# Optimization experiments

Hardware: AMD Instinct MI355X
Metric: run time of the kernel (lower is better)

Reference implementation:

```python
import jax, jax.numpy as jnp
import numpy as np

T, HID = 2048, 1536
H, DK, DV = 12, 128, 128
KEY_DIM, VAL_DIM = H * DK, H * DV
CONV_K, GEN_RED = 4, 8
EPS = 1e-5


def setup_inputs() -> dict:
    key = jax.random.key(0)
    ks = jax.random.split(key, 12)
    def rn(k, sh, scale):
        return jax.random.normal(k, sh, dtype=jnp.float32) * scale
    inv = HID ** -0.5
    return {
        "hidden_states": rn(ks[0], (T, HID), 1.0),
        "Wq": rn(ks[1], (HID, KEY_DIM), inv),
        "Wk": rn(ks[2], (HID, KEY_DIM), inv),
        "Wv": rn(ks[3], (HID, VAL_DIM), inv),
        "Wb": rn(ks[4], (HID, H), inv),
        "Wa": rn(ks[5], (HID, H), inv),
        "A_log": jnp.log(jax.random.uniform(ks[6], (H,), minval=1e-3, maxval=16.0)),
        "dt_bias": jnp.ones((H,), jnp.float32),
        "Wg1": rn(ks[7], (HID, HID // GEN_RED), inv),
        "Wg2": rn(ks[8], (HID // GEN_RED, VAL_DIM * CONV_K), (HID // GEN_RED) ** -0.5),
        "Wgate": rn(ks[9], (HID, VAL_DIM), inv),
        "norm_weight": jnp.ones((DV,), jnp.float32),
        "Wo": rn(ks[10], (VAL_DIM, HID), VAL_DIM ** -0.5),
    }


def _dynamic_conv(v, hs, Wg1, Wg2):
    # per-token per-channel causal depthwise conv; kernels generated from hidden_states
    w = jax.nn.silu(hs @ Wg1) @ Wg2                    # (T, VAL_DIM*K)
    w = w.reshape(T, VAL_DIM, CONV_K)                  # (T, D, K)
    vpad = jnp.pad(v, ((CONV_K - 1, 0), (0, 0)))       # causal left pad
    windows = jnp.stack([vpad[i:i + T] for i in range(CONV_K)], axis=1)  # (T, K, D)
    return jax.nn.silu(jnp.einsum('tkd,tdk->td', windows, w))


def _gated_delta_rule(q, k, v, g, beta):
    # q,k: (T,H,DK); v: (T,H,DV); g,beta: (T,H)
    scale = DK ** -0.5
    def step(S, inp):
        q_t, k_t, v_t, g_t, b_t = inp
        S = S * jnp.exp(g_t)[:, None, None]            # decay state
        kv = jnp.einsum('hk,hkv->hv', k_t, S)          # k^T S
        S = S + jnp.einsum('hk,hv->hkv', k_t, (v_t - kv) * b_t[:, None])
        o_t = jnp.einsum('hk,hkv->hv', q_t, S) * scale
        return S, o_t
    S0 = jnp.zeros((H, DK, DV), jnp.float32)
    _, o = jax.lax.scan(step, S0, (q, k, v, g, beta))
    return o                                           # (T, H, DV)


def reference(hidden_states, Wq, Wk, Wv, Wb, Wa, A_log, dt_bias,
              Wg1, Wg2, Wgate, norm_weight, Wo):
    hs = hidden_states
    q = jax.nn.silu(hs @ Wq).reshape(T, H, DK)
    k = jax.nn.silu(hs @ Wk).reshape(T, H, DK)
    v = _dynamic_conv(hs @ Wv, hs, Wg1, Wg2).reshape(T, H, DV)
    beta = jax.nn.sigmoid(hs @ Wb)                           # (T, H)
    g = -jnp.exp(A_log) * jax.nn.softplus(hs @ Wa + dt_bias)  # (T, H) log-decay
    o = _gated_delta_rule(q, k, v, g, beta)                  # (T, H, DV)
    # gated RMSNorm over head_v_dim
    gate = (hs @ Wgate).reshape(T, H, DV)
    o = o * jax.lax.rsqrt(jnp.mean(o * o, axis=-1, keepdims=True) + EPS)
    o = o * norm_weight * (gate * jax.nn.sigmoid(gate))
    return o.reshape(T, VAL_DIM) @ Wo
```

## Files before the change

kernel.cpp:

```cpp
#include <hip/hip_runtime.h>
#include <hip/hip_bf16.h>
#include <math.h>

#define T     2048
#define HID   1536
#define NH    12
#define DK    128
#define DV    128
#define CONVK 4
#define CH    64
#define NC    32

typedef __attribute__((ext_vector_type(8))) short bf16x8;
typedef __attribute__((ext_vector_type(8))) _Float16 fp16x8;
typedef __attribute__((ext_vector_type(4))) float floatx4;

__device__ __forceinline__ float siluf(float x) {
    return x / (1.0f + __expf(-x));
}
__device__ __forceinline__ unsigned short f2bf(float f) {
    union { __hip_bfloat16 b; unsigned short u; } cv;
    cv.b = __float2bfloat16(f);
    return cv.u;
}
__device__ __forceinline__ float bf2f(unsigned short u) {
    union { unsigned int u; float f; } cv;
    cv.u = ((unsigned int)u) << 16;
    return cv.f;
}
__device__ __forceinline__ unsigned short f2h(float f) {
    union { _Float16 h; unsigned short u; } cv;
    cv.h = (_Float16)f;
    return cv.u;
}
__device__ __forceinline__ void gl_lds16(const void* g, void* l) {
    __builtin_amdgcn_global_load_lds(
        (const __attribute__((address_space(1))) void*)g,
        (__attribute__((address_space(3))) void*)l, 16, 0, 0);
}
__device__ __forceinline__ void split8_store(const float* xv,
                                             unsigned short* dh, unsigned short* dl) {
    ushort4 h0, h1, l0, l1;
    h0.x = f2bf(xv[0]); l0.x = f2bf(xv[0] - bf2f(h0.x));
    h0.y = f2bf(xv[1]); l0.y = f2bf(xv[1] - bf2f(h0.y));
    h0.z = f2bf(xv[2]); l0.z = f2bf(xv[2] - bf2f(h0.z));
    h0.w = f2bf(xv[3]); l0.w = f2bf(xv[3] - bf2f(h0.w));
    h1.x = f2bf(xv[4]); l1.x = f2bf(xv[4] - bf2f(h1.x));
    h1.y = f2bf(xv[5]); l1.y = f2bf(xv[5] - bf2f(h1.y));
    h1.z = f2bf(xv[6]); l1.z = f2bf(xv[6] - bf2f(h1.z));
    h1.w = f2bf(xv[7]); l1.w = f2bf(xv[7] - bf2f(h1.w));
    *(ushort4*)dh = h0; *(ushort4*)(dh + 4) = h1;
    *(ushort4*)dl = l0; *(ushort4*)(dl + 4) = l1;
}

__global__ __launch_bounds__(256) void splitcast3_kernel(const float* __restrict__ s,
                                                         unsigned short* __restrict__ hi,
                                                         unsigned short* __restrict__ lo,
                                                         unsigned short* __restrict__ h16,
                                                         int n4) {
    int i = blockIdx.x * 256 + threadIdx.x;
    if (i >= n4) return;
    float4 x = ((const float4*)s)[i];
    ushort4 h, l, f;
    h.x = f2bf(x.x); l.x = f2bf(x.x - bf2f(h.x)); f.x = f2h(x.x);
    h.y = f2bf(x.y); l.y = f2bf(x.y - bf2f(h.y)); f.y = f2h(x.y);
    h.z = f2bf(x.z); l.z = f2bf(x.z - bf2f(h.z)); f.z = f2h(x.z);
    h.w = f2bf(x.w); l.w = f2bf(x.w - bf2f(h.w)); f.w = f2h(x.w);
    ((ushort4*)hi)[i] = h;
    ((ushort4*)lo)[i] = l;
    ((ushort4*)h16)[i] = f;
}

__global__ __launch_bounds__(256) void transsplit_kernel(const float* __restrict__ src,
                                                         unsigned short* __restrict__ hi,
                                                         unsigned short* __restrict__ lo,
                                                         int K, int N) {
    __shared__ float tile[32][33];
    const int k0 = blockIdx.y * 32, n0 = blockIdx.x * 32;
    const int tx = threadIdx.x, ty = threadIdx.y;
#pragma unroll
    for (int r = 0; r < 4; ++r) {
        int kk = k0 + ty + 8 * r, nn = n0 + tx;
        tile[ty + 8 * r][tx] = (nn < N) ? src[(size_t)kk * N + nn] : 0.0f;
    }
    __syncthreads();
#pragma unroll
    for (int r = 0; r < 4; ++r) {
        int nn = n0 + ty + 8 * r, kk = k0 + tx;
        if (nn < N) {
            float x = tile[tx][ty + 8 * r];
            unsigned short h = f2bf(x);
            hi[(size_t)nn * K + kk] = h;
            lo[(size_t)nn * K + kk] = f2bf(x - bf2f(h));
        }
    }
}

__global__ __launch_bounds__(256) void transcasth_kernel(const float* __restrict__ src,
                                                         unsigned short* __restrict__ dst,
                                                         int K, int N) {
    __shared__ float tile[32][33];
    const int k0 = blockIdx.y * 32, n0 = blockIdx.x * 32;
    const int tx = threadIdx.x, ty = threadIdx.y;
#pragma unroll
    for (int r = 0; r < 4; ++r) {
        int kk = k0 + ty + 8 * r, nn = n0 + tx;
        tile[ty + 8 * r][tx] = (nn < N) ? src[(size_t)kk * N + nn] : 0.0f;
    }
    __syncthreads();
#pragma unroll
    for (int r = 0; r < 4; ++r) {
        int nn = n0 + ty + 8 * r, kk = k0 + tx;
        if (nn < N) dst[(size_t)nn * K + kk] = f2h(tile[tx][ty + 8 * r]);
    }
}

template<int EPI, int MODE>
__global__ __launch_bounds__(256)
void mgemm(const unsigned short* __restrict__ Ah, const unsigned short* __restrict__ Al,
           const unsigned short* __restrict__ Bh, const unsigned short* __restrict__ Bl,
           int K, int N, float* __restrict__ C, unsigned short* __restrict__ Cb,
           float* __restrict__ qf, float* __restrict__ vf, float* __restrict__ kf,
           unsigned short* __restrict__ gsilb, unsigned short* __restrict__ w1h16,
           float* __restrict__ bgraw)
{
    constexpr int BN   = MODE ? 64 : 128;
    constexpr int BCH  = BN / 16;
    constexpr int NFR  = MODE ? 2 : 4;
    __shared__ unsigned short AsH[2][4096];
    __shared__ unsigned short BsH[2][BCH * 512];
    __shared__ unsigned short AsL[MODE ? 2 : 1][MODE ? 4096 : 4];
    __shared__ unsigned short BsL[MODE ? 2 : 1][MODE ? BCH * 512 : 4];
    const int tid = threadIdx.x;
    const int wave = tid >> 6, lane = tid & 63;
    const int wr = wave >> 1, wc = wave & 1;
    const int lm = lane & 15, lq = lane >> 4;
    const int rowBase = blockIdx.y * 128, colBase = blockIdx.x * BN;

    floatx4 acc[4][NFR];
#pragma unroll
    for (int i = 0; i < 4; ++i)
#pragma unroll
        for (int j = 0; j < NFR; ++j) acc[i][j] = (floatx4){0.f, 0.f, 0.f, 0.f};

    const int mt0 = wave * 2, mt1 = wave * 2 + 1;
    const size_t aOff0 = (size_t)(rowBase + mt0 * 16 + lm) * K + lq * 8;
    const size_t aOff1 = (size_t)(rowBase + mt1 * 16 + lm) * K + lq * 8;
    const size_t bOff0 = (size_t)(colBase + mt0 * 16 + lm) * K + lq * 8;
    const size_t bOff1 = (size_t)(colBase + mt1 * 16 + lm) * K + lq * 8;
    const size_t bOffW = (size_t)(colBase + wave * 16 + lm) * K + lq * 8;

    auto STAGE = [&](int buf, int k0) {
        gl_lds16(Ah + aOff0 + k0, &AsH[buf][mt0 * 512]);
        gl_lds16(Ah + aOff1 + k0, &AsH[buf][mt1 * 512]);
        if (MODE) {
            gl_lds16(Al + aOff0 + k0, &AsL[buf][mt0 * 512]);
            gl_lds16(Al + aOff1 + k0, &AsL[buf][mt1 * 512]);
            gl_lds16(Bh + bOffW + k0, &BsH[buf][wave * 512]);
            gl_lds16(Bl + bOffW + k0, &BsL[buf][wave * 512]);
        } else {
            gl_lds16(Bh + bOff0 + k0, &BsH[buf][mt0 * 512]);
            gl_lds16(Bh + bOff1 + k0, &BsH[buf][mt1 * 512]);
        }
    };

    const int nIter = K >> 5;
    STAGE(0, 0);
    __syncthreads();
    int cur = 0;
    for (int it = 0; it < nIter; ++it) {
        if (it + 1 < nIter) STAGE(cur ^ 1, (it + 1) << 5);
        if (MODE == 0) {
            fp16x8 a[4], b[4];
#pragma unroll
            for (int i = 0; i < 4; ++i) {
                a[i] = *(const fp16x8*)&AsH[cur][(wr * 4 + i) * 512 + lane * 8];
                b[i] = *(const fp16x8*)&BsH[cur][(wc * 4 + i) * 512 + lane * 8];
            }
#pragma unroll
            for (int mi = 0; mi < 4; ++mi)
#pragma unroll
                for (int ni = 0; ni < 4; ++ni)
                    acc[mi][ni] = __builtin_amdgcn_mfma_f32_16x16x32_f16(
                        a[mi], b[ni], acc[mi][ni], 0, 0, 0);
        } else {
            bf16x8 ah[4], al[4], bh[2], bl[2];
#pragma unroll
            for (int i = 0; i < 4; ++i) {
                ah[i] = *(const bf16x8*)&AsH[cur][(wr * 4 + i) * 512 + lane * 8];
                al[i] = *(const bf16x8*)&AsL[cur][(wr * 4 + i) * 512 + lane * 8];
            }
#pragma unroll
            for (int j = 0; j < 2; ++j) {
                bh[j] = *(const bf16x8*)&BsH[cur][(wc * 2 + j) * 512 + lane * 8];
                bl[j] = *(const bf16x8*)&BsL[cur][(wc * 2 + j) * 512 + lane * 8];
            }
#pragma unroll
            for (int mi = 0; mi < 4; ++mi)
#pragma unroll
                for (int ni = 0; ni < 2; ++ni) {
                    acc[mi][ni] = __builtin_amdgcn_mfma_f32_16x16x32_bf16(
                        ah[mi], bh[ni], acc[mi][ni], 0, 0, 0);
                    acc[mi][ni] = __builtin_amdgcn_mfma_f32_16x16x32_bf16(
                        al[mi], bh[ni], acc[mi][ni], 0, 0, 0);
                    acc[mi][ni] = __builtin_amdgcn_mfma_f32_16x16x32_bf16(
                        ah[mi], bl[ni], acc[mi][ni], 0, 0, 0);
                }
        }
        __syncthreads();
        cur ^= 1;
    }

#pragma unroll
    for (int mi = 0; mi < 4; ++mi)
#pragma unroll
        for (int ni = 0; ni < NFR; ++ni) {
            const int col = colBase + wc * (NFR * 16) + ni * 16 + lm;
#pragma unroll
            for (int r = 0; r < 4; ++r) {
                const int row = rowBase + wr * 64 + mi * 16 + lq * 4 + r;
                const float x = acc[mi][ni][r];
                if (EPI == 0) {
                    C[(size_t)row * N + col] = x;
                } else if (EPI == 3) {
                    Cb[(size_t)row * N + col] = f2bf(x);
                } else if (EPI == 1) {
                    if (col < 1536)       qf[(size_t)row * 1536 + col] = siluf(x);
                    else if (col < 3072)  vf[(size_t)row * 1536 + col - 1536] = x;
                    else if (col < 4608)  gsilb[(size_t)row * 1536 + col - 3072] = f2bf(siluf(x));
                    else if (col < 4800)  w1h16[(size_t)row * 192 + col - 4608] = f2h(siluf(x));
                } else {
                    if (col < 1536)       kf[(size_t)row * 1536 + col] = siluf(x);
                    else if (col < 1560)  bgraw[(size_t)row * 24 + col - 1536] = x;
                }
            }
        }
}

__global__ __launch_bounds__(256) void bg2_kernel(const float* __restrict__ bgraw,
                                                  const float* __restrict__ A_log,
                                                  const float* __restrict__ dt_bias,
                                                  float* __restrict__ beta,
                                                  float* __restrict__ g) {
    int idx = blockIdx.x * 256 + threadIdx.x;
    if (idx >= T * 24) return;
    int t = idx / 24, c = idx % 24;
    float x = bgraw[idx];
    if (c < 12) {
        beta[t * NH + c] = 1.0f / (1.0f + __expf(-x));
    } else {
        int h = c - 12;
        float y = x + dt_bias[h];
        float sp = (y > 20.0f) ? y : log1pf(__expf(y));
        g[t * NH + h] = -__expf(A_log[h]) * sp;
    }
}

__global__ __launch_bounds__(256) void conv_kernel(const float* __restrict__ vpre,
                                                   const unsigned short* __restrict__ w,
                                                   float* __restrict__ v) {
    const int idx = blockIdx.x * 256 + threadIdx.x;
    if (idx >= T * HID) return;
    const int t = idx / HID, d = idx % HID;
    const ushort4 wv = *(const ushort4*)(w + (size_t)t * (HID * CONVK) + d * 4);
    const float w4[4] = { bf2f(wv.x), bf2f(wv.y), bf2f(wv.z), bf2f(wv.w) };
    float acc = 0.0f;
#pragma unroll
    for (int i = 0; i < CONVK; i++) {
        const int ts = t - (CONVK - 1) + i;
        if (ts >= 0) acc += vpre[(size_t)ts * HID + d] * w4[i];
    }
    v[idx] = siluf(acc);
}

__global__ __launch_bounds__(256) void prep_kernel(
    const float* __restrict__ q, const float* __restrict__ k,
    unsigned short* __restrict__ Qth, unsigned short* __restrict__ Qtl,
    unsigned short* __restrict__ Kth, unsigned short* __restrict__ Ktl)
{
    __shared__ float KT[128 * 68];
    const int c = blockIdx.x, h = blockIdx.y;
    const int tid = threadIdx.x;
    const size_t tb = (size_t)(h * NC + c) * 8192;

    {
        const int li = tid >> 2, lq4 = tid & 3;
        const float* src = k + (size_t)(c * CH + li) * HID + h * DK + lq4 * 32;
#pragma unroll
        for (int f = 0; f < 8; ++f) {
            float4 x = *(const float4*)(src + f * 4);
            int d0 = lq4 * 32 + f * 4;
            KT[(d0 + 0) * 68 + li] = x.x; KT[(d0 + 1) * 68 + li] = x.y;
            KT[(d0 + 2) * 68 + li] = x.z; KT[(d0 + 3) * 68 + li] = x.w;
        }
    }

#pragma unroll
    for (int e = 0; e < 4; ++e) {
        int u = e * 256 + tid;
        int ch = u >> 6, l = u & 63;
        int i = (ch >> 2) * 16 + (l & 15);
        int dbase = (ch & 3) * 32 + (l >> 4) * 8;
        const float* src = q + (size_t)(c * CH + i) * HID + h * DK + dbase;
        float4 a = *(const float4*)src, b = *(const float4*)(src + 4);
        float xv[8] = {a.x, a.y, a.z, a.w, b.x, b.y, b.z, b.w};
        split8_store(xv, &Qth[tb + ch * 512 + l * 8], &Qtl[tb + ch * 512 + l * 8]);
    }
    __syncthreads();

#pragma unroll
    for (int e = 0; e < 4; ++e) {
        int u = e * 256 + tid;
        int ch = u >> 6, l = u & 63;
        int dk = (ch >> 1) * 16 + (l & 15);
        int ibase = (ch & 1) * 32 + (l >> 4) * 8;
        float4 a = *(const float4*)&KT[dk * 68 + ibase];
        float4 b = *(const float4*)&KT[dk * 68 + ibase + 4];
        float xv[8] = {a.x, a.y, a.z, a.w, b.x, b.y, b.z, b.w};
        split8_store(xv, &Kth[tb + ch * 512 + l * 8], &Ktl[tb + ch * 512 + l * 8]);
    }
}

__global__ __launch_bounds__(256, 1) void chunkloc_kernel(
    const float* __restrict__ q, const float* __restrict__ k, const float* __restrict__ v,
    const float* __restrict__ g, const float* __restrict__ beta,
    float* __restrict__ X1g,
    unsigned short* __restrict__ X2th, unsigned short* __restrict__ X2tl,
    float* __restrict__ Mg, float* __restrict__ csg)
{
    __shared__ unsigned short KhS[64 * 136], KlS[64 * 136];
    __shared__ unsigned short QhS[64 * 136], QlS[64 * 136];
    __shared__ float KT[128 * 68];
    __shared__ float Vs[64 * 132];
    __shared__ float As[64 * 68];
    __shared__ float cs[64], sb[64], sbb[64];

    const int c = blockIdx.x, h = blockIdx.y;
    const int tid = threadIdx.x;
    const int wave = tid >> 6, lane = tid & 63;
    const int lm = lane & 15, lq = lane >> 4;
    const int li = tid >> 2, lq4 = tid & 3;
    const size_t rowbase = (size_t)(c * CH) * HID + h * DK;

    {
        const float* ksrc = k + rowbase + (size_t)li * HID + lq4 * 32;
        const float* qsrc = q + rowbase + (size_t)li * HID + lq4 * 32;
        const float* vsrc = v + (size_t)(c * CH + li) * HID + h * DV + lq4 * 32;
#pragma unroll
        for (int f = 0; f < 8; ++f) {
            float4 kx = *(const float4*)(ksrc + f * 4);
            float4 qx = *(const float4*)(qsrc + f * 4);
            float4 vx = *(const float4*)(vsrc + f * 4);
            const int d0 = lq4 * 32 + f * 4;
            {
                ushort4 hh, ll;
                hh.x = f2bf(kx.x); ll.x = f2bf(kx.x - bf2f(hh.x));
                hh.y = f2bf(kx.y); ll.y = f2bf(kx.y - bf2f(hh.y));
                hh.z = f2bf(kx.z); ll.z = f2bf(kx.z - bf2f(hh.z));
                hh.w = f2bf(kx.w); ll.w = f2bf(kx.w - bf2f(hh.w));
                *(ushort4*)&KhS[li * 136 + d0] = hh;
                *(ushort4*)&KlS[li * 136 + d0] = ll;
            }
            {
                ushort4 hh, ll;
                hh.x = f2bf(qx.x); ll.x = f2bf(qx.x - bf2f(hh.x));
                hh.y = f2bf(qx.y); ll.y = f2bf(qx.y - bf2f(hh.y));
                hh.z = f2bf(qx.z); ll.z = f2bf(qx.z - bf2f(hh.z));
                hh.w = f2bf(qx.w); ll.w = f2bf(qx.w - bf2f(hh.w));
                *(ushort4*)&QhS[li * 136 + d0] = hh;
                *(ushort4*)&QlS[li * 136 + d0] = ll;
            }
            KT[(d0 + 0) * 68 + li] = kx.x;
            KT[(d0 + 1) * 68 + li] = kx.y;
            KT[(d0 + 2) * 68 + li] = kx.z;
            KT[(d0 + 3) * 68 + li] = kx.w;
            *(float4*)&Vs[li * 132 + d0] = vx;
        }
    }
    if (tid < 64) {
        float gv = g[(c * CH + tid) * NH + h];
        float bv = beta[(c * CH + tid) * NH + h];
        float csv = gv;
#pragma unroll
        for (int off = 1; off < 64; off <<= 1) {
            float n = __shfl_up(csv, off);
            if (tid >= off) csv += n;
        }
        cs[tid] = csv; sb[tid] = bv; sbb[tid] = bv * __expf(csv);
    }
    __syncthreads();

    {
        const int ti = wave;
#pragma unroll
        for (int tj = 0; tj < 4; ++tj) {
            floatx4 acc = (floatx4){0.f, 0.f, 0.f, 0.f};
#pragma unroll
            for (int ks = 0; ks < 4; ++ks) {
                bf16x8 a_h = *(const bf16x8*)&KhS[(ti * 16 + lm) * 136 + ks * 32 + lq * 8];
                bf16x8 a_l = *(const bf16x8*)&KlS[(ti * 16 + lm) * 136 + ks * 32 + lq * 8];
                bf16x8 b_h = *(const bf16x8*)&KhS[(tj * 16 + lm) * 136 + ks * 32 + lq * 8];
                bf16x8 b_l = *(const bf16x8*)&KlS[(tj * 16 + lm) * 136 + ks * 32 + lq * 8];
                acc = __builtin_amdgcn_mfma_f32_16x16x32_bf16(a_h, b_h, acc, 0, 0, 0);
                acc = __builtin_amdgcn_mfma_f32_16x16x32_bf16(a_h, b_l, acc, 0, 0, 0);
                acc = __builtin_amdgcn_mfma_f32_16x16x32_bf16(a_l, b_h, acc, 0, 0, 0);
            }
#pragma unroll
            for (int r = 0; r < 4; ++r) {
                const int i = ti * 16 + lq * 4 + r, j = tj * 16 + lm;
                As[i * 68 + j] = (j < i) ? sb[i] * __expf(cs[i] - cs[j]) * acc[r] : 0.0f;
            }
        }
        const size_t mbase = (size_t)(h * NC + c) * CH * CH;
#pragma unroll
        for (int tj = 0; tj < 4; ++tj) {
            floatx4 acc = (floatx4){0.f, 0.f, 0.f, 0.f};
#pragma unroll
            for (int ks = 0; ks < 4; ++ks) {
                bf16x8 a_h = *(const bf16x8*)&QhS[(ti * 16 + lm) * 136 + ks * 32 + lq * 8];
                bf16x8 a_l = *(const bf16x8*)&QlS[(ti * 16 + lm) * 136 + ks * 32 + lq * 8];
                bf16x8 b_h = *(const bf16x8*)&KhS[(tj * 16 + lm) * 136 + ks * 32 + lq * 8];
                bf16x8 b_l = *(const bf16x8*)&KlS[(tj * 16 + lm) * 136 + ks * 32 + lq * 8];
                acc = __builtin_amdgcn_mfma_f32_16x16x32_bf16(a_h, b_h, acc, 0, 0, 0);
                acc = __builtin_amdgcn_mfma_f32_16x16x32_bf16(a_h, b_l, acc, 0, 0, 0);
                acc = __builtin_amdgcn_mfma_f32_16x16x32_bf16(a_l, b_h, acc, 0, 0, 0);
            }
#pragma unroll
            for (int r = 0; r < 4; ++r) {
                const int i = ti * 16 + lq * 4 + r, j = tj * 16 + lm;
                Mg[mbase + (size_t)i * 64 + j] =
                    (j <= i) ? __expf(cs[i] - cs[j]) * acc[r] : 0.0f;
            }
        }
    }

    float xc[64];
    const int col = tid;
    if (col < 128) {
#pragma unroll
        for (int i = 0; i < 64; ++i) xc[i] = sb[i] * Vs[i * 132 + col];
    } else {
        const int dcol = col - 128;
#pragma unroll
        for (int i4 = 0; i4 < 16; ++i4) {
            float4 kq = *(const float4*)&KT[dcol * 68 + i4 * 4];
            xc[i4 * 4 + 0] = sbb[i4 * 4 + 0] * kq.x;
            xc[i4 * 4 + 1] = sbb[i4 * 4 + 1] * kq.y;
            xc[i4 * 4 + 2] = sbb[i4 * 4 + 2] * kq.z;
            xc[i4 * 4 + 3] = sbb[i4 * 4 + 3] * kq.w;
        }
    }
    __syncthreads();

#pragma unroll
    for (int i = 1; i < 64; ++i) {
        float a = xc[i];
#pragma unroll
        for (int j4 = 0; j4 < (i + 3) / 4; ++j4) {
            float4 a4 = *(const float4*)&As[i * 68 + j4 * 4];
            a -= a4.x * xc[j4 * 4 + 0] + a4.y * xc[j4 * 4 + 1]
               + a4.z * xc[j4 * 4 + 2] + a4.w * xc[j4 * 4 + 3];
        }
        xc[i] = a;
    }

    {
        const size_t xbase = (size_t)(h * NC + c) * CH * 128;
        if (col < 128) {
            for (int i = 0; i < 64; ++i) X1g[xbase + (size_t)i * 128 + col] = xc[i];
        } else {
            for (int i = 0; i < 64; ++i) Vs[i * 132 + (col - 128)] = xc[i];
        }
    }
    if (tid < 64) csg[(size_t)(h * NC + c) * CH + tid] = cs[tid];
    __syncthreads();

    {
        const size_t tb = (size_t)(h * NC + c) * 8192;
#pragma unroll
        for (int e = 0; e < 4; ++e) {
            int u = e * 256 + tid;
            int ch = u >> 6, l = u & 63;
            int i = (ch >> 2) * 16 + (l & 15);
            int dbase = (ch & 3) * 32 + (l >> 4) * 8;
            float4 a = *(const float4*)&Vs[i * 132 + dbase];
            float4 b = *(const float4*)&Vs[i * 132 + dbase + 4];
            float xv[8] = {-a.x, -a.y, -a.z, -a.w, -b.x, -b.y, -b.z, -b.w};
            split8_store(xv, &X2th[tb + ch * 512 + l * 8], &X2tl[tb + ch * 512 + l * 8]);
        }
    }
}

struct StFrags {
    bf16x8 xh[4], xl[4], qh[4], ql[4], kh[4], kl[4];
    float x1r[4], csr[4], cs63;
};

__device__ __forceinline__ void st_load(
    StFrags& f,
    const unsigned short* __restrict__ Qth, const unsigned short* __restrict__ Qtl,
    const unsigned short* __restrict__ Kth, const unsigned short* __restrict__ Ktl,
    const unsigned short* __restrict__ X2th, const unsigned short* __restrict__ X2tl,
    const float* __restrict__ X1g, const float* __restrict__ csg,
    int h, int c, int db, int mw, int lane, int lq, int lm)
{
    const size_t hc = (size_t)(h * NC + c);
    const size_t xb = hc * CH * 128;
    const size_t tb = hc * 8192 + (size_t)lane * 8;
#pragma unroll
    for (int ks = 0; ks < 4; ++ks) {
        const size_t off = tb + (size_t)(mw * 4 + ks) * 512;
        f.xh[ks] = *(const bf16x8*)(X2th + off);
        f.xl[ks] = *(const bf16x8*)(X2tl + off);
        f.qh[ks] = *(const bf16x8*)(Qth + off);
        f.ql[ks] = *(const bf16x8*)(Qtl + off);
        f.kh[ks] = *(const bf16x8*)(Kth + off);
        f.kl[ks] = *(const bf16x8*)(Ktl + off);
    }
#pragma unroll
    for (int r = 0; r < 4; ++r) {
        const int row = mw * 16 + lq * 4 + r;
        f.x1r[r] = X1g[xb + (size_t)row * 128 + db * 16 + lm];
        f.csr[r] = csg[hc * CH + row];
    }
    f.cs63 = csg[hc * CH + 63];
}

__device__ __forceinline__ void st_compute(
    const StFrags& f, floatx4& st0, floatx4& st1,
    unsigned short* SBh, unsigned short* SBl,
    unsigned short* UBh, unsigned short* UBl,
    float* __restrict__ X1g, float* __restrict__ o,
    int h, int c, int db, int mw, int lane, int lq, int lm)
{
    const size_t hc = (size_t)(h * NC + c);
    const size_t xb = hc * CH * 128;

    {
        floatx4 aU0 = (floatx4){0.f, 0.f, 0.f, 0.f};
        floatx4 aU1 = (floatx4){0.f, 0.f, 0.f, 0.f};
        floatx4 aO0 = (floatx4){0.f, 0.f, 0.f, 0.f};
        floatx4 aO1 = (floatx4){0.f, 0.f, 0.f, 0.f};
#pragma unroll
        for (int ks = 0; ks < 4; ++ks) {
            bf16x8 sh = *(const bf16x8*)&SBh[lm * 136 + ks * 32 + lq * 8];
            bf16x8 sl = *(const bf16x8*)&SBl[lm * 136 + ks * 32 + lq * 8];
            if (ks & 1) {
                aU1 = __builtin_amdgcn_mfma_f32_16x16x32_bf16(f.xh[ks], sh, aU1, 0, 0, 0);
                aU1 = __builtin_amdgcn_mfma_f32_16x16x32_bf16(f.xh[ks], sl, aU1, 0, 0, 0);
                aU1 = __builtin_amdgcn_mfma_f32_16x16x32_bf16(f.xl[ks], sh, aU1, 0, 0, 0);
                aO1 = __builtin_amdgcn_mfma_f32_16x16x32_bf16(f.qh[ks], sh, aO1, 0, 0, 0);
                aO1 = __builtin_amdgcn_mfma_f32_16x16x32_bf16(f.qh[ks], sl, aO1, 0, 0, 0);
                aO1 = __builtin_amdgcn_mfma_f32_16x16x32_bf16(f.ql[ks], sh, aO1, 0, 0, 0);
            } else {
                aU0 = __builtin_amdgcn_mfma_f32_16x16x32_bf16(f.xh[ks], sh, aU0, 0, 0, 0);
                aU0 = __builtin_amdgcn_mfma_f32_16x16x32_bf16(f.xh[ks], sl, aU0, 0, 0, 0);
                aU0 = __builtin_amdgcn_mfma_f32_16x16x32_bf16(f.xl[ks], sh, aU0, 0, 0, 0);
                aO0 = __builtin_amdgcn_mfma_f32_16x16x32_bf16(f.qh[ks], sh, aO0, 0, 0, 0);
                aO0 = __builtin_amdgcn_mfma_f32_16x16x32_bf16(f.qh[ks], sl, aO0, 0, 0, 0);
                aO0 = __builtin_amdgcn_mfma_f32_16x16x32_bf16(f.ql[ks], sh, aO0, 0, 0, 0);
            }
        }
#pragma unroll
        for (int r = 0; r < 4; ++r) {
            const int row = mw * 16 + lq * 4 + r;
            const float u = aU0[r] + aU1[r] + f.x1r[r];
            X1g[xb + (size_t)row * 128 + db * 16 + lm] = u;
            const float up = u * __expf(f.cs63 - f.csr[r]);
            unsigned short uh = f2bf(up);
            UBh[lm * 72 + row] = uh;
            UBl[lm * 72 + row] = f2bf(up - bf2f(uh));
            o[(size_t)(c * CH + row) * HID + h * DV + db * 16 + lm] =
                __expf(f.csr[r]) * (aO0[r] + aO1[r]);
        }
    }
    __syncthreads();

    {
        const float bC = __expf(f.cs63);
#pragma unroll
        for (int mt2 = 0; mt2 < 2; ++mt2) {
            const int mt = mw * 2 + mt2;
            floatx4 acc;
            floatx4 stc = mt2 ? st1 : st0;
#pragma unroll
            for (int r = 0; r < 4; ++r) acc[r] = bC * stc[r];
#pragma unroll
            for (int ks = 0; ks < 2; ++ks) {
                bf16x8 ah = f.kh[mt2 * 2 + ks];
                bf16x8 al = f.kl[mt2 * 2 + ks];
                bf16x8 bh = *(const bf16x8*)&UBh[lm * 72 + ks * 32 + lq * 8];
                bf16x8 bl = *(const bf16x8*)&UBl[lm * 72 + ks * 32 + lq * 8];
                acc = __builtin_amdgcn_mfma_f32_16x16x32_bf16(ah, bh, acc, 0, 0, 0);
                acc = __builtin_amdgcn_mfma_f32_16x16x32_bf16(ah, bl, acc, 0, 0, 0);
                acc = __builtin_amdgcn_mfma_f32_16x16x32_bf16(al, bh, acc, 0, 0, 0);
            }
            if (mt2) st1 = acc; else st0 = acc;
            ushort4 shv, slv;
#pragma unroll
            for (int r = 0; r < 4; ++r) {
                const float sv = acc[r];
                unsigned short sh = f2bf(sv);
                ((unsigned short*)&shv)[r] = sh;
                ((unsigned short*)&slv)[r] = f2bf(sv - bf2f(sh));
            }
            const int dkb = mt * 16 + lq * 4;
            *(ushort4*)&SBh[lm * 136 + dkb] = shv;
            *(ushort4*)&SBl[lm * 136 + dkb] = slv;
        }
    }
    __syncthreads();
}

__global__ __launch_bounds__(256, 1) void state_kernel(
    const unsigned short* __restrict__ Qth, const unsigned short* __restrict__ Qtl,
    const unsigned short* __restrict__ Kth, const unsigned short* __restrict__ Ktl,
    const unsigned short* __restrict__ X2th, const unsigned short* __restrict__ X2tl,
    float* __restrict__ X1g ,
    const float* __restrict__ csg, float* __restrict__ o)
{
    __shared__ unsigned short SBh[16 * 136], SBl[16 * 136];
    __shared__ unsigned short UBh[16 * 72],  UBl[16 * 72];

    const int h = blockIdx.x, db = blockIdx.y;
    const int tid = threadIdx.x;
    const int mw = tid >> 6, lane = tid & 63;
    const int lm = lane & 15, lq = lane >> 4;

    for (int idx = tid; idx < 16 * 136; idx += 256) { SBh[idx] = 0; SBl[idx] = 0; }
    floatx4 st0 = (floatx4){0.f, 0.f, 0.f, 0.f};
    floatx4 st1 = (floatx4){0.f, 0.f, 0.f, 0.f};
    __syncthreads();

    StFrags fA, fB;
    st_load(fA, Qth, Qtl, Kth, Ktl, X2th, X2tl, X1g, csg, h, 0, db, mw, lane, lq, lm);
    for (int c = 0; c < NC; c += 2) {
        st_load(fB, Qth, Qtl, Kth, Ktl, X2th, X2tl, X1g, csg, h, c + 1, db, mw, lane, lq, lm);
        __builtin_amdgcn_sched_barrier(0);
        st_compute(fA, st0, st1, SBh, SBl, UBh, UBl, X1g, o, h, c, db, mw, lane, lq, lm);
        if (c + 2 < NC)
            st_load(fA, Qth, Qtl, Kth, Ktl, X2th, X2tl, X1g, csg, h, c + 2, db, mw, lane, lq, lm);
        __builtin_amdgcn_sched_barrier(0);
        st_compute(fB, st0, st1, SBh, SBl, UBh, UBl, X1g, o, h, c + 1, db, mw, lane, lq, lm);
    }
}

__global__ __launch_bounds__(256) void outk_kernel(
    const float* __restrict__ Ug, const float* __restrict__ Mg,
    float* __restrict__ o)
{
    __shared__ float Msh[64 * 68];
    __shared__ float Ush[64 * 68];

    const int c = blockIdx.x, h = blockIdx.y;
    const int dvb = blockIdx.z * 64;
    const int tid = threadIdx.x;
    const size_t hc = (size_t)(h * NC + c);

    for (int e = 0; e < 16; ++e) {
        int idx = e * 256 + tid;
        Msh[(idx >> 6) * 68 + (idx & 63)] = Mg[hc * CH * CH + idx];
    }
    for (int e = 0; e < 16; ++e) {
        int idx = e * 256 + tid;
        int j = idx >> 6, cc = idx & 63;
        Ush[j * 68 + cc] = Ug[hc * CH * 128 + (size_t)j * 128 + dvb + cc];
    }
    __syncthreads();

    const int tx = tid & 15, ty = tid >> 4;
    const int c0 = tx * 4, i0 = ty * 4;
    float acc[4][4] = {{0}};
    for (int j4 = 0; j4 < 16; ++j4) {
        float uv[4][4];
#pragma unroll
        for (int s = 0; s < 4; ++s) {
            float4 u4 = *(const float4*)&Ush[(j4 * 4 + s) * 68 + c0];
            uv[s][0] = u4.x; uv[s][1] = u4.y; uv[s][2] = u4.z; uv[s][3] = u4.w;
        }
#pragma unroll
        for (int r = 0; r < 4; ++r) {
            float4 m4 = *(const float4*)&Msh[(i0 + r) * 68 + j4 * 4];
            const float mv[4] = {m4.x, m4.y, m4.z, m4.w};
#pragma unroll
            for (int s = 0; s < 4; ++s)
#pragma unroll
                for (int e = 0; e < 4; ++e) acc[r][e] += mv[s] * uv[s][e];
        }
    }
    const float scale = 0.08838834764831845f;
#pragma unroll
    for (int r = 0; r < 4; ++r) {
        float* op = &o[(size_t)(c * CH + i0 + r) * HID + h * DV + dvb + c0];
        float4 prev = *(const float4*)op;
        float4 ov = make_float4(scale * (prev.x + acc[r][0]),
                                scale * (prev.y + acc[r][1]),
                                scale * (prev.z + acc[r][2]),
                                scale * (prev.w + acc[r][3]));
        *(float4*)op = ov;
    }
}

__global__ __launch_bounds__(256) void normgate_kernel(const float* __restrict__ o,
                                                       const unsigned short* __restrict__ gsil,
                                                       const float* __restrict__ nw,
                                                       unsigned short* __restrict__ out_hi,
                                                       unsigned short* __restrict__ out_lo) {
    const int gw = (blockIdx.x * 256 + threadIdx.x) >> 6;
    const int lane = threadIdx.x & 63;
    if (gw >= T * NH) return;
    const int t = gw / NH, h = gw % NH;
    const size_t base = (size_t)t * HID + h * DV;
    const float a = o[base + lane];
    const float b = o[base + lane + 64];
    float ss = a * a + b * b;
    ss += __shfl_xor(ss, 1);  ss += __shfl_xor(ss, 2);  ss += __shfl_xor(ss, 4);
    ss += __shfl_xor(ss, 8);  ss += __shfl_xor(ss, 16); ss += __shfl_xor(ss, 32);
    const float r = rsqrtf(ss * (1.0f / 128.0f) + 1e-5f);
    float va = a * r * nw[lane]      * bf2f(gsil[base + lane]);
    float vb = b * r * nw[lane + 64] * bf2f(gsil[base + lane + 64]);
    unsigned short ha = f2bf(va), hb = f2bf(vb);
    out_hi[base + lane]      = ha;  out_lo[base + lane]      = f2bf(va - bf2f(ha));
    out_hi[base + lane + 64] = hb;  out_lo[base + lane + 64] = f2bf(vb - bf2f(hb));
}

extern "C" void kernel_launch(void* const* d_in, const int* in_sizes, int n_in,
                              void* d_out, int out_size, void* d_ws, size_t ws_size,
                              hipStream_t stream) {
    const float* hs      = (const float*)d_in[0];
    const float* Wq      = (const float*)d_in[1];
    const float* Wk      = (const float*)d_in[2];
    const float* Wv      = (const float*)d_in[3];
    const float* Wb      = (const float*)d_in[4];
    const float* Wa      = (const float*)d_in[5];
    const float* A_log   = (const float*)d_in[6];
    const float* dt_bias = (const float*)d_in[7];
    const float* Wg1     = (const float*)d_in[8];
    const float* Wg2     = (const float*)d_in[9];
    const float* Wgate   = (const float*)d_in[10];
    const float* norm_w  = (const float*)d_in[11];
    const float* Wo      = (const float*)d_in[12];

    float* ws = (float*)d_ws;
    float* q    = ws;
    float* kbuf = ws + 3145728;
    float* vpre = ws + 6291456;
    float* vbuf = ws + 9437184;
    unsigned short* gsil = (unsigned short*)(ws + 12582912);
    float* X1g  = ws + 14155776;
    unsigned short* X2th = (unsigned short*)(ws + 17301504);
    unsigned short* X2tl = (unsigned short*)(ws + 18874368);
    float* Mg   = ws + 20447232;
    unsigned short* WTAfh = (unsigned short*)(ws + 14155776);
    unsigned short* WTBh  = (unsigned short*)(ws + 17891328);
    unsigned short* WTBl  = (unsigned short*)(ws + 19169280);
    unsigned short* wcv   = (unsigned short*)(ws + 14155776);
    unsigned short* WG2h  = (unsigned short*)(ws + 22044672);
    unsigned short* hsh   = (unsigned short*)(ws + 22634496);
    unsigned short* w1h16 = (unsigned short*)(ws + 24207360);
    float* bgraw = ws + 24403968;
    unsigned short* Kth = (unsigned short*)(ws + 22044672);
    unsigned short* Ktl = (unsigned short*)(ws + 23617536);
    float* beta  = ws + 25190400;
    float* g     = ws + 25214976;
    float* csg   = ws + 25239552;
    unsigned short* hsbh = (unsigned short*)(ws + 9437184);
    unsigned short* hsbl = (unsigned short*)(ws + 11010048);
    unsigned short* Qth  = (unsigned short*)(ws + 6291456);
    unsigned short* Qtl  = (unsigned short*)(ws + 7864320);
    unsigned short* WoTh = (unsigned short*)(ws);
    unsigned short* WoTl = (unsigned short*)(ws + 1179648);
    unsigned short* onh  = (unsigned short*)(ws + 6291456);
    unsigned short* onl  = (unsigned short*)(ws + 7864320);

    const dim3 blk(256);
    const dim3 blkT(32, 8);

    splitcast3_kernel<<<3072, blk, 0, stream>>>(hs, hsbh, hsbl, hsh, (T * HID) / 4);
    transcasth_kernel<<<dim3(48, 48), blkT, 0, stream>>>(Wq,    WTAfh,               1536, 1536);
    transcasth_kernel<<<dim3(48, 48), blkT, 0, stream>>>(Wv,    WTAfh + 1536 * 1536, 1536, 1536);
    transcasth_kernel<<<dim3(48, 48), blkT, 0, stream>>>(Wgate, WTAfh + 3072 * 1536, 1536, 1536);
    transcasth_kernel<<<dim3(6, 48),  blkT, 0, stream>>>(Wg1,   WTAfh + 4608 * 1536, 1536, 192);
    transsplit_kernel<<<dim3(48, 48), blkT, 0, stream>>>(Wk, WTBh,               WTBl,               1536, 1536);
    transsplit_kernel<<<dim3(1, 48),  blkT, 0, stream>>>(Wb, WTBh + 1536 * 1536, WTBl + 1536 * 1536, 1536, 12);
    transsplit_kernel<<<dim3(1, 48),  blkT, 0, stream>>>(Wa, WTBh + 1548 * 1536, WTBl + 1548 * 1536, 1536, 12);
    transcasth_kernel<<<dim3(192, 6), blkT, 0, stream>>>(Wg2, WG2h, 192, 6144);

    mgemm<1, 0><<<dim3(38, 16), blk, 0, stream>>>(hsh, nullptr, WTAfh, nullptr, 1536, 4864,
        nullptr, nullptr, q, vpre, nullptr, gsil, w1h16, nullptr);
    mgemm<2, 1><<<dim3(26, 16), blk, 0, stream>>>(hsbh, hsbl, WTBh, WTBl, 1536, 1664,
        nullptr, nullptr, nullptr, nullptr, kbuf, nullptr, nullptr, bgraw);
    bg2_kernel<<<192, blk, 0, stream>>>(bgraw, A_log, dt_bias, beta, g);

    mgemm<3, 0><<<dim3(48, 16), blk, 0, stream>>>(w1h16, nullptr, WG2h, nullptr, 192, 6144,
        nullptr, wcv, nullptr, nullptr, nullptr, nullptr, nullptr, nullptr);
    conv_kernel<<<(T * HID) / 256, blk, 0, stream>>>(vpre, wcv, vbuf);

    chunkloc_kernel<<<dim3(NC, NH), blk, 0, stream>>>(q, kbuf, vbuf, g, beta,
                                                      X1g, X2th, X2tl, Mg, csg);
    prep_kernel<<<dim3(NC, NH), blk, 0, stream>>>(q, kbuf, Qth, Qtl, Kth, Ktl);
    state_kernel<<<dim3(NH, 8), blk, 0, stream>>>(Qth, Qtl, Kth, Ktl, X2th, X2tl,
                                                  X1g, csg, vbuf);
    transsplit_kernel<<<dim3(48, 48), blkT, 0, stream>>>(Wo, WoTh, WoTl, 1536, 1536);
    outk_kernel<<<dim3(NC, NH, 2), blk, 0, stream>>>(X1g, Mg, vbuf);

    normgate_kernel<<<6144, blk, 0, stream>>>(vbuf, gsil, norm_w, onh, onl);
    mgemm<0, 1><<<dim3(24, 16), blk, 0, stream>>>(onh, onl, WoTh, WoTl, 1536, 1536,
        (float*)d_out, nullptr, nullptr, nullptr, nullptr, nullptr, nullptr, nullptr);
}
```

Measured before the change: 544.6 us.

## Merge the two input-projection GEMMs into one interleaved launch

The fp16 projection GEMM (q/v/gate/Wg1) and the split-bf16 projection GEMM (k/beta/a) become one kernel with a 1-D grid of 1024 blocks. Even and odd blocks take roles from the two GEMMs until the smaller one is used up, and the remaining blocks finish the larger one. The aim is to cut one launch and the tail of each GEMM so both fill the CUs together. Shared memory is sized for the larger role, which may lower occupancy for the fp16 role.

```diff
diff --git a/kernel.cpp b/kernel.cpp
--- a/kernel.cpp
+++ b/kernel.cpp
@@ -119,10 +119,7 @@
 __global__ __launch_bounds__(256)
 void mgemm(const unsigned short* __restrict__ Ah, const unsigned short* __restrict__ Al,
            const unsigned short* __restrict__ Bh, const unsigned short* __restrict__ Bl,
-           int K, int N, float* __restrict__ C, unsigned short* __restrict__ Cb,
-           float* __restrict__ qf, float* __restrict__ vf, float* __restrict__ kf,
-           unsigned short* __restrict__ gsilb, unsigned short* __restrict__ w1h16,
-           float* __restrict__ bgraw)
+           int K, int N, float* __restrict__ C, unsigned short* __restrict__ Cb)
 {
     constexpr int BN   = MODE ? 64 : 128;
     constexpr int BCH  = BN / 16;
@@ -220,21 +217,158 @@
             for (int r = 0; r < 4; ++r) {
                 const int row = rowBase + wr * 64 + mi * 16 + lq * 4 + r;
                 const float x = acc[mi][ni][r];
-                if (EPI == 0) {
-                    C[(size_t)row * N + col] = x;
-                } else if (EPI == 3) {
-                    Cb[(size_t)row * N + col] = f2bf(x);
-                } else if (EPI == 1) {
+                if (EPI == 0) C[(size_t)row * N + col] = x;
+                else          Cb[(size_t)row * N + col] = f2bf(x);
+            }
+        }
+}
+
+__global__ __launch_bounds__(256)
+void mgemm_ab(const unsigned short* __restrict__ Ah0, const unsigned short* __restrict__ Bh0,
+              const unsigned short* __restrict__ Ah1, const unsigned short* __restrict__ Al1,
+              const unsigned short* __restrict__ Bh1, const unsigned short* __restrict__ Bl1,
+              float* __restrict__ qf, float* __restrict__ vf,
+              unsigned short* __restrict__ gsilb, unsigned short* __restrict__ w1h16,
+              float* __restrict__ kf, float* __restrict__ bgraw)
+{
+    __shared__ unsigned short smem[24576];
+    const int tid = threadIdx.x;
+    const int wave = tid >> 6, lane = tid & 63;
+    const int wr = wave >> 1, wc = wave & 1;
+    const int lm = lane & 15, lq = lane >> 4;
+    const int K = 1536;
+    const int bx = blockIdx.x;
+
+    bool roleA; int aidx = 0, bidx = 0;
+    if (bx < 832) { roleA = ((bx & 1) == 0); aidx = bx >> 1; bidx = bx >> 1; }
+    else          { roleA = true;            aidx = 416 + (bx - 832); }
+
+    const int mt0 = wave * 2, mt1 = wave * 2 + 1;
+
+    if (roleA) {
+        const int rowBase = (aidx / 38) * 128, colBase = (aidx % 38) * 128;
+        unsigned short* AsH = smem;
+        unsigned short* BsH = smem + 8192;
+        floatx4 acc[4][4];
+#pragma unroll
+        for (int i = 0; i < 4; ++i)
+#pragma unroll
+            for (int j = 0; j < 4; ++j) acc[i][j] = (floatx4){0.f, 0.f, 0.f, 0.f};
+
+        const size_t aOff0 = (size_t)(rowBase + mt0 * 16 + lm) * K + lq * 8;
+        const size_t aOff1 = (size_t)(rowBase + mt1 * 16 + lm) * K + lq * 8;
+        const size_t bOff0 = (size_t)(colBase + mt0 * 16 + lm) * K + lq * 8;
+        const size_t bOff1 = (size_t)(colBase + mt1 * 16 + lm) * K + lq * 8;
+
+        auto STAGE = [&](int buf, int k0) {
+            gl_lds16(Ah0 + aOff0 + k0, &AsH[buf * 4096 + mt0 * 512]);
+            gl_lds16(Ah0 + aOff1 + k0, &AsH[buf * 4096 + mt1 * 512]);
+            gl_lds16(Bh0 + bOff0 + k0, &BsH[buf * 4096 + mt0 * 512]);
+            gl_lds16(Bh0 + bOff1 + k0, &BsH[buf * 4096 + mt1 * 512]);
+        };
+        STAGE(0, 0);
+        __syncthreads();
+        int cur = 0;
+        for (int it = 0; it < 48; ++it) {
+            if (it + 1 < 48) STAGE(cur ^ 1, (it + 1) << 5);
+            fp16x8 a[4], b[4];
+#pragma unroll
+            for (int i = 0; i < 4; ++i) {
+                a[i] = *(const fp16x8*)&AsH[cur * 4096 + (wr * 4 + i) * 512 + lane * 8];
+                b[i] = *(const fp16x8*)&BsH[cur * 4096 + (wc * 4 + i) * 512 + lane * 8];
+            }
+#pragma unroll
+            for (int mi = 0; mi < 4; ++mi)
+#pragma unroll
+                for (int ni = 0; ni < 4; ++ni)
+                    acc[mi][ni] = __builtin_amdgcn_mfma_f32_16x16x32_f16(
+                        a[mi], b[ni], acc[mi][ni], 0, 0, 0);
+            __syncthreads();
+            cur ^= 1;
+        }
+#pragma unroll
+        for (int mi = 0; mi < 4; ++mi)
+#pragma unroll
+            for (int ni = 0; ni < 4; ++ni) {
+                const int col = colBase + wc * 64 + ni * 16 + lm;
+#pragma unroll
+                for (int r = 0; r < 4; ++r) {
+                    const int row = rowBase + wr * 64 + mi * 16 + lq * 4 + r;
+                    const float x = acc[mi][ni][r];
                     if (col < 1536)       qf[(size_t)row * 1536 + col] = siluf(x);
                     else if (col < 3072)  vf[(size_t)row * 1536 + col - 1536] = x;
                     else if (col < 4608)  gsilb[(size_t)row * 1536 + col - 3072] = f2bf(siluf(x));
                     else if (col < 4800)  w1h16[(size_t)row * 192 + col - 4608] = f2h(siluf(x));
-                } else {
+                }
+            }
+    } else {
+        const int rowBase = (bidx / 26) * 128, colBase = (bidx % 26) * 64;
+        unsigned short* AsH = smem;
+        unsigned short* AsL = smem + 8192;
+        unsigned short* BsH = smem + 16384;
+        unsigned short* BsL = smem + 20480;
+        floatx4 acc[4][2];
+#pragma unroll
+        for (int i = 0; i < 4; ++i)
+#pragma unroll
+            for (int j = 0; j < 2; ++j) acc[i][j] = (floatx4){0.f, 0.f, 0.f, 0.f};
+
+        const size_t aOff0 = (size_t)(rowBase + mt0 * 16 + lm) * K + lq * 8;
+        const size_t aOff1 = (size_t)(rowBase + mt1 * 16 + lm) * K + lq * 8;
+        const size_t bOffW = (size_t)(colBase + wave * 16 + lm) * K + lq * 8;
+
+        auto STAGE = [&](int buf, int k0) {
+            gl_lds16(Ah1 + aOff0 + k0, &AsH[buf * 4096 + mt0 * 512]);
+            gl_lds16(Ah1 + aOff1 + k0, &AsH[buf * 4096 + mt1 * 512]);
+            gl_lds16(Al1 + aOff0 + k0, &AsL[buf * 4096 + mt0 * 512]);
+            gl_lds16(Al1 + aOff1 + k0, &AsL[buf * 4096 + mt1 * 512]);
+            gl_lds16(Bh1 + bOffW + k0, &BsH[buf * 2048 + wave * 512]);
+            gl_lds16(Bl1 + bOffW + k0, &BsL[buf * 2048 + wave * 512]);
+        };
+        STAGE(0, 0);
+        __syncthreads();
+        int cur = 0;
+        for (int it = 0; it < 48; ++it) {
+            if (it + 1 < 48) STAGE(cur ^ 1, (it + 1) << 5);
+            bf16x8 ah[4], al[4], bh[2], bl[2];
+#pragma unroll
+            for (int i = 0; i < 4; ++i) {
+                ah[i] = *(const bf16x8*)&AsH[cur * 4096 + (wr * 4 + i) * 512 + lane * 8];
+                al[i] = *(const bf16x8*)&AsL[cur * 4096 + (wr * 4 + i) * 512 + lane * 8];
+            }
+#pragma unroll
+            for (int j = 0; j < 2; ++j) {
+                bh[j] = *(const bf16x8*)&BsH[cur * 2048 + (wc * 2 + j) * 512 + lane * 8];
+                bl[j] = *(const bf16x8*)&BsL[cur * 2048 + (wc * 2 + j) * 512 + lane * 8];
+            }
+#pragma unroll
+            for (int mi = 0; mi < 4; ++mi)
+#pragma unroll
+                for (int ni = 0; ni < 2; ++ni) {
+                    acc[mi][ni] = __builtin_amdgcn_mfma_f32_16x16x32_bf16(
+                        ah[mi], bh[ni], acc[mi][ni], 0, 0, 0);
+                    acc[mi][ni] = __builtin_amdgcn_mfma_f32_16x16x32_bf16(
+                        al[mi], bh[ni], acc[mi][ni], 0, 0, 0);
+                    acc[mi][ni] = __builtin_amdgcn_mfma_f32_16x16x32_bf16(
+                        ah[mi], bl[ni], acc[mi][ni], 0, 0, 0);
+                }
+            __syncthreads();
+            cur ^= 1;
+        }
+#pragma unroll
+        for (int mi = 0; mi < 4; ++mi)
+#pragma unroll
+            for (int ni = 0; ni < 2; ++ni) {
+                const int col = colBase + wc * 32 + ni * 16 + lm;
+#pragma unroll
+                for (int r = 0; r < 4; ++r) {
+                    const int row = rowBase + wr * 64 + mi * 16 + lq * 4 + r;
+                    const float x = acc[mi][ni][r];
                     if (col < 1536)       kf[(size_t)row * 1536 + col] = siluf(x);
                     else if (col < 1560)  bgraw[(size_t)row * 24 + col - 1536] = x;
                 }
             }
-        }
+    }
 }
 
 __global__ __launch_bounds__(256) void bg2_kernel(const float* __restrict__ bgraw,
@@ -786,14 +920,12 @@
     transsplit_kernel<<<dim3(1, 48),  blkT, 0, stream>>>(Wa, WTBh + 1548 * 1536, WTBl + 1548 * 1536, 1536, 12);
     transcasth_kernel<<<dim3(192, 6), blkT, 0, stream>>>(Wg2, WG2h, 192, 6144);
 
-    mgemm<1, 0><<<dim3(38, 16), blk, 0, stream>>>(hsh, nullptr, WTAfh, nullptr, 1536, 4864,
-        nullptr, nullptr, q, vpre, nullptr, gsil, w1h16, nullptr);
-    mgemm<2, 1><<<dim3(26, 16), blk, 0, stream>>>(hsbh, hsbl, WTBh, WTBl, 1536, 1664,
-        nullptr, nullptr, nullptr, nullptr, kbuf, nullptr, nullptr, bgraw);
+    mgemm_ab<<<1024, blk, 0, stream>>>(hsh, WTAfh, hsbh, hsbl, WTBh, WTBl,
+                                       q, vpre, gsil, w1h16, kbuf, bgraw);
     bg2_kernel<<<192, blk, 0, stream>>>(bgraw, A_log, dt_bias, beta, g);
 
     mgemm<3, 0><<<dim3(48, 16), blk, 0, stream>>>(w1h16, nullptr, WG2h, nullptr, 192, 6144,
-        nullptr, wcv, nullptr, nullptr, nullptr, nullptr, nullptr, nullptr);
+        nullptr, wcv);
     conv_kernel<<<(T * HID) / 256, blk, 0, stream>>>(vpre, wcv, vbuf);
 
     chunkloc_kernel<<<dim3(NC, NH), blk, 0, stream>>>(q, kbuf, vbuf, g, beta,
@@ -806,5 +938,5 @@
 
     normgate_kernel<<<6144, blk, 0, stream>>>(vbuf, gsil, norm_w, onh, onl);
     mgemm<0, 1><<<dim3(24, 16), blk, 0, stream>>>(onh, onl, WoTh, WoTl, 1536, 1536,
-        (float*)d_out, nullptr, nullptr, nullptr, nullptr, nullptr, nullptr, nullptr);
-}
+        (float*)d_out, nullptr);
+}
```

Result: no change. 539.7 us (-0.9%).
